# Optimization experiments

Hardware: AMD Instinct MI355X
Metric: run time of the kernel (lower is better)

Reference implementation:

```python
import jax, jax.numpy as jnp
from jax import lax
import numpy as np

B, CIN, HC, K, REC = 64, 64, 64, 3, 5
MG = 240 // REC  # 48
EPS = 1e-8


def conv2d(x, w, b, pad):
    y = lax.conv_general_dilated(x, w, (1, 1), [(pad, pad), (pad, pad)],
                                 dimension_numbers=('NCHW', 'OIHW', 'NCHW'))
    return y + b[None, :, None, None]


def conv_transpose2d(x, w, b, stride, pad):
    # PyTorch ConvTranspose2d: w is (Cin, Cout, kH, kW)
    k = w.shape[2]
    w_t = jnp.transpose(w[:, :, ::-1, ::-1], (1, 0, 2, 3))  # -> OIHW, flipped
    y = lax.conv_general_dilated(x, w_t, (1, 1),
                                 [(k - 1 - pad, k - 1 - pad)] * 2,
                                 lhs_dilation=(stride, stride),
                                 dimension_numbers=('NCHW', 'OIHW', 'NCHW'))
    return y + b[None, :, None, None]


def leaky(x):
    return jnp.where(x >= 0, x, 0.2 * x)


def setup_inputs() -> dict:
    key = jax.random.key(0)
    ks = jax.random.split(key, 12)
    s = 0.05
    return {
        'x': jax.random.normal(ks[0], (B, CIN, 64, 64), jnp.float32),
        'h': jax.random.normal(ks[1], (B, HC, 64, 64), jnp.float32),
        'c': jax.random.normal(ks[2], (B, HC, 64, 64), jnp.float32),
        'recalled_memory_feature': jax.random.normal(ks[3], (B, REC, MG, 32, 32), jnp.float32),
        'conv_w': jax.random.normal(ks[4], (5 * HC, CIN + HC, K, K), jnp.float32) * s,
        'conv_b': jax.random.normal(ks[5], (5 * HC,), jnp.float32) * s,
        'convc_w': jax.random.normal(ks[6], (MG, HC, 1, 1), jnp.float32) * s,
        'convc_b': jax.random.normal(ks[7], (MG,), jnp.float32) * s,
        'convssm_w': jax.random.normal(ks[8], (MG, MG, 4, 4), jnp.float32) * s,
        'convssm_b': jax.random.normal(ks[9], (MG,), jnp.float32) * s,
        'convfuse_w': jax.random.normal(ks[10], (HC, MG + HC, 1, 1), jnp.float32) * s,
        'convfuse_b': jax.random.normal(ks[11], (HC,), jnp.float32) * s,
    }


def reference(x, h, c, recalled_memory_feature, conv_w, conv_b, convc_w, convc_b,
              convssm_w, convssm_b, convfuse_w, convfuse_b):
    rm = recalled_memory_feature.reshape(B, REC, MG, 32, 32)
    rm_avg = rm.mean(axis=(3, 4))                      # (B, REC, MG)
    q = leaky(conv2d(c, convc_w, convc_b, 0))          # (B, MG, 64, 64)
    q_avg = q.mean(axis=(2, 3))                        # (B, MG)
    # cosine similarity along channel dim, vectorized over (B, REC)
    qn = jnp.maximum(jnp.linalg.norm(q_avg, axis=1, keepdims=True), EPS)   # (B,1)
    mn = jnp.maximum(jnp.linalg.norm(rm_avg, axis=2), EPS)                  # (B,REC)
    cos = jnp.einsum('bm,brm->br', q_avg, rm_avg) / (qn * mn)               # (B,REC)
    attn = jax.nn.softmax(cos, axis=1)                                      # (B,REC)
    mt = jnp.einsum('br,brmhw->bmhw', attn, rm)        # (B, MG, 32, 32)
    mt = leaky(conv_transpose2d(mt, convssm_w, convssm_b, 2, 1))  # (B, MG, 64, 64)

    gates = conv2d(jnp.concatenate((x, h), axis=1), conv_w, conv_b, K // 2)
    i, f, g, o, lam = jnp.split(gates, 5, axis=1)
    i = jax.nn.sigmoid(i)
    f = jax.nn.sigmoid(f)
    o = jax.nn.sigmoid(o)
    g = jnp.tanh(g)
    lam = jax.nn.sigmoid(lam)
    c_new = f * c + i * g
    h_new = o * jnp.tanh(conv2d(jnp.concatenate((c_new, mt), axis=1), convfuse_w, convfuse_b, 0))
    h_out = lam * h_new + (1.0 - lam) * h
    return (h_out, c_new)
```

## Files before the change

### kernel.cpp

```cpp
#include <hip/hip_runtime.h>
#include <hip/hip_bf16.h>
#include <cstdint>

#define HW 4096
#define MGc 48
#define RECc 5

typedef __attribute__((ext_vector_type(8))) short bf16x8;
typedef __attribute__((ext_vector_type(4))) float f32x4;

__device__ __forceinline__ float sigf(float x) { return 1.f / (1.f + expf(-x)); }
__device__ __forceinline__ float leakyf(float x) { return x >= 0.f ? x : 0.2f * x; }
__device__ __forceinline__ unsigned short f2bfu(float f) {
  __hip_bfloat16 b = __float2bfloat16(f);
  return *reinterpret_cast<unsigned short*>(&b);
}
__device__ __forceinline__ float bfu2f(unsigned short u) {
  unsigned v = ((unsigned)u) << 16;
  return __uint_as_float(v);
}
__device__ __forceinline__ void gload_lds16(const void* g, void* l) {
  __builtin_amdgcn_global_load_lds(
      (const __attribute__((address_space(1))) unsigned int*)g,
      (__attribute__((address_space(3))) unsigned int*)l, 16, 0, 0);
}

__global__ __launch_bounds__(256) void k_att(const float* __restrict__ rm,
    float* __restrict__ rm_sum, const float* __restrict__ c,
    const float* __restrict__ ccw, const float* __restrict__ ccb,
    float* __restrict__ q_part) {
  __shared__ __align__(16) char smem[13568];
  int bid = blockIdx.x, tid = threadIdx.x;
  if (bid < 15360) {
    float* sred = (float*)smem;
    int row = bid;
    const float4* p = reinterpret_cast<const float4*>(rm + (size_t)row * 1024);
    float4 v = p[tid];
    float s = v.x + v.y + v.z + v.w;
    #pragma unroll
    for (int off = 32; off; off >>= 1) s += __shfl_down(s, off);
    if ((tid & 63) == 0) sred[tid >> 6] = s;
    __syncthreads();
    if (tid == 0) rm_sum[row] = sred[0] + sred[1] + sred[2] + sred[3];
  } else {
    float* wl = (float*)smem;
    float* bl = wl + MGc * 64;
    float (*red)[MGc] = (float(*)[MGc])(bl + 64);
    int r = bid - 15360;
    int seg = r & 15, b = r >> 4;
    for (int i = tid; i < MGc * 64; i += 256) wl[i] = ccw[i];
    if (tid < MGc) bl[tid] = ccb[tid];
    __syncthreads();
    int px = seg * 256 + tid;
    float acc[MGc];
    #pragma unroll
    for (int m = 0; m < MGc; m++) acc[m] = 0.f;
    const float* cp = c + (size_t)b * 64 * HW + px;
    for (int ci = 0; ci < 64; ci++) {
      float v = cp[(size_t)ci * HW];
      #pragma unroll
      for (int m = 0; m < MGc; m++) acc[m] += wl[m * 64 + ci] * v;
    }
    int lane = tid & 63, wv = tid >> 6;
    #pragma unroll
    for (int m = 0; m < MGc; m++) {
      float t2 = leakyf(acc[m] + bl[m]);
      #pragma unroll
      for (int off = 32; off; off >>= 1) t2 += __shfl_down(t2, off);
      if (lane == 0) red[wv][m] = t2;
    }
    __syncthreads();
    if (tid < MGc) {
      float t2 = red[0][tid] + red[1][tid] + red[2][tid] + red[3][tid];
      q_part[((size_t)b * 16 + seg) * MGc + tid] = t2;
    }
  }
}

__global__ __launch_bounds__(256) void k_mid(const float* __restrict__ rm,
    const float* __restrict__ rm_sum, const float* __restrict__ q_part,
    float* __restrict__ mt_pre, const float* __restrict__ cw,
    __hip_bfloat16* __restrict__ Wp, __hip_bfloat16* __restrict__ Pp,
    const float* __restrict__ xin, const float* __restrict__ hin) {
  __shared__ __align__(16) char smem[16704];
  int bid = blockIdx.x, tid = threadIdx.x;
  if (bid < 12288) {
    float* sat = (float*)smem;
    int idx = bid * 256 + tid;
    int b = idx / (MGc * 1024);
    if (tid < 64) {
      int lane = tid;
      float q = 0.f;
      if (lane < MGc) {
        float s = 0.f;
        for (int sg = 0; sg < 16; sg++) s += q_part[((size_t)b * 16 + sg) * MGc + lane];
        q = s * (1.f / 4096.f);
      }
      float qs = q * q;
      #pragma unroll
      for (int off = 32; off; off >>= 1) qs += __shfl_xor(qs, off);
      float qn = fmaxf(sqrtf(qs), 1e-8f);
      float cosv[RECc];
      #pragma unroll
      for (int r = 0; r < RECc; r++) {
        float m = 0.f;
        if (lane < MGc) m = rm_sum[((size_t)b * RECc + r) * MGc + lane] * (1.f / 1024.f);
        float d = q * m, ms = m * m;
        #pragma unroll
        for (int off = 32; off; off >>= 1) { d += __shfl_xor(d, off); ms += __shfl_xor(ms, off); }
        float mn = fmaxf(sqrtf(ms), 1e-8f);
        cosv[r] = d / (qn * mn);
      }
      float mx = cosv[0];
      #pragma unroll
      for (int r = 1; r < RECc; r++) mx = fmaxf(mx, cosv[r]);
      float ssum = 0.f;
      #pragma unroll
      for (int r = 0; r < RECc; r++) { cosv[r] = expf(cosv[r] - mx); ssum += cosv[r]; }
      float inv = 1.f / ssum;
      #pragma unroll
      for (int r = 0; r < RECc; r++)
        if (lane == r) sat[r] = cosv[r] * inv;
    }
    __syncthreads();
    int rem = idx - b * (MGc * 1024);
    const float* base = rm + (size_t)b * RECc * MGc * 1024 + rem;
    float v = sat[0] * base[0] + sat[1] * base[MGc * 1024] + sat[2] * base[2 * MGc * 1024]
            + sat[3] * base[3 * MGc * 1024] + sat[4] * base[4 * MGc * 1024];
    mt_pre[idx] = v;
  } else if (bid < 13728) {
    int idx = (bid - 12288) * 256 + tid;
    int t = idx / (320 * 128);
    int rem = idx % (320 * 128);
    int ocp = rem / 128, ci = rem % 128;
    int nt = ocp / 80, r2 = ocp % 80, gate = r2 / 16, ml = r2 % 16;
    int oc = gate * 64 + nt * 16 + ml;
    Wp[idx] = __float2bfloat16(cw[((size_t)oc * 128 + ci) * 9 + t]);
  } else if (bid < 14768) {
    int idx = (bid - 13728) * 256 + tid;
    int b = idx / 4160, i = idx % 4160;
    bf16x8* base = reinterpret_cast<bf16x8*>(Pp);
    size_t u;
    if (i < 2112) {
      int r = (i < 1056) ? 0 : 65;
      int j = (i < 1056) ? i : i - 1056;
      u = ((size_t)b * 66 + r) * 1056 + j;
    } else {
      int i2 = i - 2112;
      int row = 1 + (i2 >> 5), k = i2 & 31;
      int px = (k < 16) ? 0 : 65, ci8 = k & 15;
      u = (((size_t)b * 66 + row) * 66 + px) * 16 + ci8;
    }
    base[u] = (bf16x8)0;
  } else {
    float (*t)[65] = (float(*)[65])smem;
    int r = bid - 14768;
    int half = r & 1, y = (r >> 1) & 63, b = r >> 7;
    const float* src = (half ? hin : xin) + (size_t)b * 64 * HW + y * 64;
    #pragma unroll
    for (int it = 0; it < 4; it++) {
      int li = it * 256 + tid;
      int ci = li >> 4, x4 = (li & 15) * 4;
      float4 v = *reinterpret_cast<const float4*>(src + (size_t)ci * HW + x4);
      t[x4][ci] = v.x; t[x4 + 1][ci] = v.y; t[x4 + 2][ci] = v.z; t[x4 + 3][ci] = v.w;
    }
    __syncthreads();
    int x = tid >> 2, c16 = (tid & 3) * 16;
    unsigned short* dst = reinterpret_cast<unsigned short*>(Pp) +
        ((((size_t)b * 66 + y + 1) * 66 + x + 1) * 128 + half * 64 + c16);
    bf16x8 o0, o1;
    #pragma unroll
    for (int j = 0; j < 8; j++) {
      o0[j] = (short)f2bfu(t[x][c16 + j]);
      o1[j] = (short)f2bfu(t[x][c16 + 8 + j]);
    }
    *reinterpret_cast<bf16x8*>(dst) = o0;
    *reinterpret_cast<bf16x8*>(dst + 8) = o1;
  }
}

__global__ __launch_bounds__(512) void k_ssm(const float* __restrict__ mt_pre,
    const float* __restrict__ w, const float* __restrict__ bias,
    __hip_bfloat16* __restrict__ mt) {
  __shared__ float in_t[12][10][20];
  __shared__ float w_t[12][48][16];
  int b = blockIdx.y;
  int tile = blockIdx.x;
  int y0 = (tile >> 1) * 16, x0 = (tile & 1) * 32;
  int wv = threadIdx.x >> 6, lane = threadIdx.x & 63;
  int co0 = wv * 6;
  int oyl = lane >> 2, xseg = lane & 3;
  int oy = y0 + oyl;
  int iy0 = (y0 >> 1) - 1, ix0 = (x0 >> 1) - 1;
  int kyA = (oy + 1) & 1;
  int iyA = (oy + 1 - kyA) >> 1;
  int rA = iyA - iy0, rB = rA - 1;
  float acc[6][8] = {};
  for (int ch = 0; ch < 4; ch++) {
    int ci0 = ch * 12;
    __syncthreads();
    for (int i = threadIdx.x; i < 12 * 10 * 18; i += 512) {
      int ci = i / 180, rr = (i % 180) / 18, cc2 = i % 18;
      int giy = iy0 + rr, gix = ix0 + cc2;
      float v = 0.f;
      if ((unsigned)giy < 32u && (unsigned)gix < 32u)
        v = mt_pre[(((size_t)b * MGc + ci0 + ci) * 32 + giy) * 32 + gix];
      in_t[ci][rr][cc2] = v;
    }
    for (int i = threadIdx.x; i < 12 * 48 * 16; i += 512)
      (&w_t[0][0][0])[i] = w[ci0 * 768 + i];
    __syncthreads();
    #pragma unroll 1
    for (int ci = 0; ci < 12; ci++) {
      float4 a0 = *reinterpret_cast<const float4*>(&in_t[ci][rA][xseg * 4]);
      float4 a1 = *reinterpret_cast<const float4*>(&in_t[ci][rA][xseg * 4 + 4]);
      float4 b0 = *reinterpret_cast<const float4*>(&in_t[ci][rB][xseg * 4]);
      float4 b1 = *reinterpret_cast<const float4*>(&in_t[ci][rB][xseg * 4 + 4]);
      float vA[6] = {a0.x, a0.y, a0.z, a0.w, a1.x, a1.y};
      float vB[6] = {b0.x, b0.y, b0.z, b0.w, b1.x, b1.y};
      #pragma unroll
      for (int co = 0; co < 6; co++) {
        const float* wp = &w_t[ci][co0 + co][0];
        float4 wA = *reinterpret_cast<const float4*>(wp + kyA * 4);
        float4 wB = *reinterpret_cast<const float4*>(wp + (kyA + 2) * 4);
        #pragma unroll
        for (int j = 0; j < 8; j++) {
          if ((j & 1) == 0) {
            int hi = (j >> 1) + 1, lo = j >> 1;
            acc[co][j] += vA[hi] * wA.y + vA[lo] * wA.w + vB[hi] * wB.y + vB[lo] * wB.w;
          } else {
            int hi = ((j + 1) >> 1) + 1, lo = (j + 1) >> 1;
            acc[co][j] += vA[hi] * wA.x + vA[lo] * wA.z + vB[hi] * wB.x + vB[lo] * wB.z;
          }
        }
      }
    }
  }
  int oxb = x0 + xseg * 8;
  #pragma unroll
  for (int co = 0; co < 6; co++) {
    float bb = bias[co0 + co];
    size_t obase = (((size_t)b * MGc + co0 + co) * 64 + oy) * 64 + oxb;
    #pragma unroll
    for (int j = 0; j < 8; j++)
      mt[obase + j] = __float2bfloat16(leakyf(acc[co][j] + bb));
  }
}

__global__ __launch_bounds__(256) void k_gates_mfma(
    const __hip_bfloat16* __restrict__ Pp, const __hip_bfloat16* __restrict__ Wp,
    const float* __restrict__ c, const float* __restrict__ cb,
    float* __restrict__ c_new, __hip_bfloat16* __restrict__ o_g,
    __hip_bfloat16* __restrict__ lam_g) {
  __shared__ bf16x8 s_in[1296];
  __shared__ bf16x8 s_w[2944];
  int orig = blockIdx.y * gridDim.x + blockIdx.x;
  int t_id = (orig & 7) * 512 + (orig >> 3);
  int b = t_id >> 6;
  int r6 = t_id & 63;
  int ytile = r6 >> 4, xtile = (r6 >> 2) & 3, nt = r6 & 3;
  int y0 = ytile * 16, x0 = xtile * 16;
  int tid = threadIdx.x;
  int wv = tid >> 6, lane = tid & 63;
  int lane15 = lane & 15, lq = lane >> 4;

  const char* Pb = (const char*)Pp;
  const char* Wb = (const char*)Wp;

  const char* gin[6]; int din[6]; bool ain[6];
  #pragma unroll
  for (int k = 0; k < 6; k++) {
    int u = wv + 4 * k;
    int e = u * 64 + lane;
    ain[k] = (u < 21) && (e < 1296);
    int ee = (e < 1296) ? e : 0;
    int L = ee / 72, r = ee - L * 72;
    int llq = r / 18, xi = r - llq * 18;
    gin[k] = Pb + ((((size_t)b * 66 + y0 + L) * 66 + (x0 + xi)) * 256) + llq * 16;
    din[k] = ee;
  }
  const char* gw[12]; int dw[12]; bool aw[12];
  #pragma unroll
  for (int k = 0; k < 12; k++) {
    int u = wv + 4 * k;
    int e = u * 64 + lane;
    aw[k] = (e < 2916);
    int ee = aw[k] ? e : 0;
    int row = ee / 81, ol = ee - row * 81;
    if (ol > 79) ol = 0;
    int t = row >> 2, g = row & 3;
    gw[k] = Wb + (((size_t)t * 320 + nt * 80 + ol) * 128 + g * 8) * 2;
    dw[k] = ee;
  }

  f32x4 acc[4][5];
  #pragma unroll
  for (int i = 0; i < 4; i++)
    #pragma unroll
    for (int j = 0; j < 5; j++) acc[i][j] = (f32x4)0.f;

  #pragma unroll 1
  for (int cc = 0; cc < 4; cc++) {
    __syncthreads();
    int co = cc * 64;
    #pragma unroll
    for (int k = 0; k < 6; k++)
      if (ain[k]) gload_lds16(gin[k] + co, (void*)&s_in[din[k]]);
    #pragma unroll
    for (int k = 0; k < 12; k++)
      if (aw[k]) gload_lds16(gw[k] + co, (void*)&s_w[dw[k]]);
    __syncthreads();

    #pragma unroll
    for (int dx = 0; dx < 3; dx++) {
      bf16x8 af[6];
      #pragma unroll
      for (int r = 0; r < 6; r++)
        af[r] = s_in[((wv * 4 + r) * 4 + lq) * 18 + lane15 + dx];
      #pragma unroll
      for (int ky = 0; ky < 3; ky++) {
        int t = ky * 3 + dx;
        bf16x8 bw[5];
        #pragma unroll
        for (int gg = 0; gg < 5; gg++)
          bw[gg] = s_w[(t * 4 + lq) * 81 + gg * 16 + lane15];
        __builtin_amdgcn_s_setprio(1);
        #pragma unroll
        for (int rr = 0; rr < 4; rr++)
          #pragma unroll
          for (int gg = 0; gg < 5; gg++)
            acc[rr][gg] = __builtin_amdgcn_mfma_f32_16x16x32_bf16(
                af[rr + ky], bw[gg], acc[rr][gg], 0, 0, 0);
        __builtin_amdgcn_s_setprio(0);
      }
    }
  }

  int m_hid = nt * 16 + lane15;
  float bi = cb[m_hid], bff = cb[64 + m_hid], bgg = cb[128 + m_hid],
        bo = cb[192 + m_hid], bl = cb[256 + m_hid];
  int xb = x0 + lq * 4;
  size_t chofs = ((size_t)b * 64 + m_hid) * HW;
  #pragma unroll
  for (int rr = 0; rr < 4; rr++) {
    int y = y0 + wv * 4 + rr;
    size_t pofs = chofs + (size_t)y * 64 + xb;
    f32x4 cold = *reinterpret_cast<const f32x4*>(c + pofs);
    f32x4 cn;
    unsigned short ov[4], lv[4];
    #pragma unroll
    for (int e = 0; e < 4; e++) {
      float i_ = sigf(acc[rr][0][e] + bi);
      float f_ = sigf(acc[rr][1][e] + bff);
      float g_ = tanhf(acc[rr][2][e] + bgg);
      float o_ = sigf(acc[rr][3][e] + bo);
      float l_ = sigf(acc[rr][4][e] + bl);
      cn[e] = f_ * cold[e] + i_ * g_;
      ov[e] = f2bfu(o_);
      lv[e] = f2bfu(l_);
    }
    *reinterpret_cast<f32x4*>(c_new + pofs) = cn;
    ushort4 ovv = {ov[0], ov[1], ov[2], ov[3]};
    ushort4 lvv = {lv[0], lv[1], lv[2], lv[3]};
    *reinterpret_cast<ushort4*>(reinterpret_cast<unsigned short*>(o_g) + pofs) = ovv;
    *reinterpret_cast<ushort4*>(reinterpret_cast<unsigned short*>(lam_g) + pofs) = lvv;
  }
}

__global__ __launch_bounds__(256) void k_fuse(const float* __restrict__ c_new,
    const __hip_bfloat16* __restrict__ mt, const __hip_bfloat16* __restrict__ o_g,
    const __hip_bfloat16* __restrict__ lam_g, const float* __restrict__ h,
    const float* __restrict__ fw, const float* __restrict__ fb,
    float* __restrict__ h_out) {
  __shared__ float wl[112][32];
  int b = blockIdx.y;
  int seg = blockIdx.x & 7, chalf = blockIdx.x >> 3;
  int co0 = chalf * 32;
  for (int i = threadIdx.x; i < 112 * 32; i += 256) {
    int ci = i >> 5, co = i & 31;
    wl[ci][co] = fw[(co0 + co) * 112 + ci];
  }
  __syncthreads();
  int px = seg * 512 + threadIdx.x * 2;
  size_t bofs = (size_t)b * 64 * HW;
  float2 acc[32];
  #pragma unroll
  for (int co = 0; co < 32; co++) { float bv = fb[co0 + co]; acc[co].x = bv; acc[co].y = bv; }
  #pragma unroll 1
  for (int ci = 0; ci < 64; ci++) {
    float2 v = *reinterpret_cast<const float2*>(c_new + bofs + (size_t)ci * HW + px);
    #pragma unroll
    for (int c4 = 0; c4 < 8; c4++) {
      float4 w = *reinterpret_cast<const float4*>(&wl[ci][c4 * 4]);
      acc[c4 * 4 + 0].x += w.x * v.x; acc[c4 * 4 + 0].y += w.x * v.y;
      acc[c4 * 4 + 1].x += w.y * v.x; acc[c4 * 4 + 1].y += w.y * v.y;
      acc[c4 * 4 + 2].x += w.z * v.x; acc[c4 * 4 + 2].y += w.z * v.y;
      acc[c4 * 4 + 3].x += w.w * v.x; acc[c4 * 4 + 3].y += w.w * v.y;
    }
  }
  const unsigned short* mtu = reinterpret_cast<const unsigned short*>(mt);
  size_t mtofs = (size_t)b * MGc * HW + px;
  #pragma unroll 1
  for (int ci = 0; ci < 48; ci++) {
    unsigned u = *reinterpret_cast<const unsigned*>(mtu + mtofs + (size_t)ci * HW);
    float vx = bfu2f((unsigned short)(u & 0xffff));
    float vy = bfu2f((unsigned short)(u >> 16));
    #pragma unroll
    for (int c4 = 0; c4 < 8; c4++) {
      float4 w = *reinterpret_cast<const float4*>(&wl[64 + ci][c4 * 4]);
      acc[c4 * 4 + 0].x += w.x * vx; acc[c4 * 4 + 0].y += w.x * vy;
      acc[c4 * 4 + 1].x += w.y * vx; acc[c4 * 4 + 1].y += w.y * vy;
      acc[c4 * 4 + 2].x += w.z * vx; acc[c4 * 4 + 2].y += w.z * vy;
      acc[c4 * 4 + 3].x += w.w * vx; acc[c4 * 4 + 3].y += w.w * vy;
    }
  }
  const unsigned short* ou = reinterpret_cast<const unsigned short*>(o_g);
  const unsigned short* lu = reinterpret_cast<const unsigned short*>(lam_g);
  #pragma unroll
  for (int co = 0; co < 32; co++) {
    size_t ofs = bofs + (size_t)(co0 + co) * HW + px;
    unsigned uo = *reinterpret_cast<const unsigned*>(ou + ofs);
    unsigned ul = *reinterpret_cast<const unsigned*>(lu + ofs);
    float2 hv = *reinterpret_cast<const float2*>(h + ofs);
    float hnx = tanhf(acc[co].x), hny = tanhf(acc[co].y);
    float ox = bfu2f((unsigned short)(uo & 0xffff)), oy = bfu2f((unsigned short)(uo >> 16));
    float lx = bfu2f((unsigned short)(ul & 0xffff)), ly = bfu2f((unsigned short)(ul >> 16));
    float2 r;
    r.x = lx * (ox * hnx) + (1.f - lx) * hv.x;
    r.y = ly * (oy * hny) + (1.f - ly) * hv.y;
    *reinterpret_cast<float2*>(h_out + ofs) = r;
  }
}

extern "C" void kernel_launch(void* const* d_in, const int* in_sizes, int n_in,
                              void* d_out, int out_size, void* d_ws, size_t ws_size,
                              hipStream_t stream) {
  const float* x   = (const float*)d_in[0];
  const float* h   = (const float*)d_in[1];
  const float* c   = (const float*)d_in[2];
  const float* rm  = (const float*)d_in[3];
  const float* cw  = (const float*)d_in[4];
  const float* cb  = (const float*)d_in[5];
  const float* ccw = (const float*)d_in[6];
  const float* ccb = (const float*)d_in[7];
  const float* sw  = (const float*)d_in[8];
  const float* sb  = (const float*)d_in[9];
  const float* fw  = (const float*)d_in[10];
  const float* fb  = (const float*)d_in[11];

  float* h_out = (float*)d_out;
  float* c_new = h_out + (size_t)16777216;

  char* ws = (char*)d_ws;
  float* rm_sum = (float*)(ws + 0);
  float* q_part = (float*)(ws + 65536);
  __hip_bfloat16* o_g   = (__hip_bfloat16*)(ws + 0);
  __hip_bfloat16* lam_g = (__hip_bfloat16*)(ws + 33554432);
  __hip_bfloat16* mt    = (__hip_bfloat16*)(ws + 67108864);
  __hip_bfloat16* Pp    = (__hip_bfloat16*)(ws + 92274688);
  __hip_bfloat16* Wp    = (__hip_bfloat16*)(ws + 163643392);
  float* mt_pre = h_out;

  k_att<<<16384, 256, 0, stream>>>(rm, rm_sum, c, ccw, ccb, q_part);
  k_mid<<<22960, 256, 0, stream>>>(rm, rm_sum, q_part, mt_pre, cw, Wp, Pp, x, h);
  k_ssm<<<dim3(8, 64), 512, 0, stream>>>(mt_pre, sw, sb, mt);
  k_gates_mfma<<<dim3(64, 64), 256, 0, stream>>>(Pp, Wp, c, cb, c_new, o_g, lam_g);
  k_fuse<<<dim3(16, 64), 256, 0, stream>>>(c_new, mt, o_g, lam_g, h, fw, fb, h_out);
}
```

Baseline: 641.4 us.

## Double-buffer gate-conv weight tiles per dx to overlap loads with MFMA

The gate convolution kernel now stages its weight tile one dx column at a time into two 960-entry LDS buffers, instead of loading all nine taps into one large buffer before computing. The global-to-LDS load for the next dx is issued before the MFMA work on the current dx, so weight loads overlap compute. This also cuts LDS use per block, which may allow more resident blocks. In exchange it adds barriers per channel chunk and drops the 81-entry padded row stride for a stride of 80, which may bring back LDS bank conflicts on the B-fragment reads.

```diff
diff --git a/kernel.cpp b/kernel.cpp
--- a/kernel.cpp
+++ b/kernel.cpp
@@ -253,7 +253,7 @@
     float* __restrict__ c_new, __hip_bfloat16* __restrict__ o_g,
     __hip_bfloat16* __restrict__ lam_g) {
   __shared__ bf16x8 s_in[1296];
-  __shared__ bf16x8 s_w[2944];
+  __shared__ bf16x8 s_w[2][960];
   int orig = blockIdx.y * gridDim.x + blockIdx.x;
   int t_id = (orig & 7) * 512 + (orig >> 3);
   int b = t_id >> 6;
@@ -279,18 +279,17 @@
     gin[k] = Pb + ((((size_t)b * 66 + y0 + L) * 66 + (x0 + xi)) * 256) + llq * 16;
     din[k] = ee;
   }
-  const char* gw[12]; int dw[12]; bool aw[12];
-  #pragma unroll
-  for (int k = 0; k < 12; k++) {
+  const char* gwb[4]; int dwb[4]; bool awb[4];
+  #pragma unroll
+  for (int k = 0; k < 4; k++) {
     int u = wv + 4 * k;
-    int e = u * 64 + lane;
-    aw[k] = (e < 2916);
-    int ee = aw[k] ? e : 0;
-    int row = ee / 81, ol = ee - row * 81;
-    if (ol > 79) ol = 0;
-    int t = row >> 2, g = row & 3;
-    gw[k] = Wb + (((size_t)t * 320 + nt * 80 + ol) * 128 + g * 8) * 2;
-    dw[k] = ee;
+    awb[k] = (u < 15);
+    int uu = awb[k] ? u : 0;
+    int e = uu * 64 + lane;
+    int row = e / 80, ol = e - row * 80;
+    int ky = row >> 2, g = row & 3;
+    gwb[k] = Wb + (((size_t)(ky * 3) * 320 + nt * 80 + ol) * 128 + g * 8) * 2;
+    dwb[k] = e;
   }
 
   f32x4 acc[4][5];
@@ -298,43 +297,55 @@
   for (int i = 0; i < 4; i++)
     #pragma unroll
     for (int j = 0; j < 5; j++) acc[i][j] = (f32x4)0.f;
+
+#define STAGE_W(BUF, DX, CO) do {                                                     \
+    _Pragma("unroll")                                                                 \
+    for (int k = 0; k < 4; k++)                                                       \
+      if (awb[k]) gload_lds16(gwb[k] + (DX) * 81920 + (CO),                           \
+                              (void*)&s_w[BUF][dwb[k]]);                              \
+  } while (0)
+
+#define COMP_DX(BUF, DX) do {                                                         \
+    bf16x8 af[6];                                                                     \
+    _Pragma("unroll")                                                                 \
+    for (int r = 0; r < 6; r++)                                                       \
+      af[r] = s_in[((wv * 4 + r) * 4 + lq) * 18 + lane15 + (DX)];                     \
+    _Pragma("unroll")                                                                 \
+    for (int ky = 0; ky < 3; ky++) {                                                  \
+      bf16x8 bw[5];                                                                   \
+      _Pragma("unroll")                                                               \
+      for (int gg = 0; gg < 5; gg++)                                                  \
+        bw[gg] = s_w[BUF][(ky * 4 + lq) * 80 + gg * 16 + lane15];                     \
+      __builtin_amdgcn_s_setprio(1);                                                  \
+      _Pragma("unroll")                                                               \
+      for (int rr = 0; rr < 4; rr++)                                                  \
+        _Pragma("unroll")                                                             \
+        for (int gg = 0; gg < 5; gg++)                                                \
+          acc[rr][gg] = __builtin_amdgcn_mfma_f32_16x16x32_bf16(                      \
+              af[rr + ky], bw[gg], acc[rr][gg], 0, 0, 0);                             \
+      __builtin_amdgcn_s_setprio(0);                                                  \
+    }                                                                                 \
+  } while (0)
 
   #pragma unroll 1
   for (int cc = 0; cc < 4; cc++) {
-    __syncthreads();
     int co = cc * 64;
+    __syncthreads();
     #pragma unroll
     for (int k = 0; k < 6; k++)
       if (ain[k]) gload_lds16(gin[k] + co, (void*)&s_in[din[k]]);
-    #pragma unroll
-    for (int k = 0; k < 12; k++)
-      if (aw[k]) gload_lds16(gw[k] + co, (void*)&s_w[dw[k]]);
-    __syncthreads();
-
-    #pragma unroll
-    for (int dx = 0; dx < 3; dx++) {
-      bf16x8 af[6];
-      #pragma unroll
-      for (int r = 0; r < 6; r++)
-        af[r] = s_in[((wv * 4 + r) * 4 + lq) * 18 + lane15 + dx];
-      #pragma unroll
-      for (int ky = 0; ky < 3; ky++) {
-        int t = ky * 3 + dx;
-        bf16x8 bw[5];
-        #pragma unroll
-        for (int gg = 0; gg < 5; gg++)
-          bw[gg] = s_w[(t * 4 + lq) * 81 + gg * 16 + lane15];
-        __builtin_amdgcn_s_setprio(1);
-        #pragma unroll
-        for (int rr = 0; rr < 4; rr++)
-          #pragma unroll
-          for (int gg = 0; gg < 5; gg++)
-            acc[rr][gg] = __builtin_amdgcn_mfma_f32_16x16x32_bf16(
-                af[rr + ky], bw[gg], acc[rr][gg], 0, 0, 0);
-        __builtin_amdgcn_s_setprio(0);
-      }
-    }
-  }
+    STAGE_W(0, 0, co);
+    __syncthreads();
+    STAGE_W(1, 1, co);
+    COMP_DX(0, 0);
+    __syncthreads();
+    STAGE_W(0, 2, co);
+    COMP_DX(1, 1);
+    __syncthreads();
+    COMP_DX(0, 2);
+  }
+#undef STAGE_W
+#undef COMP_DX
 
   int m_hid = nt * 16 + lane15;
   float bi = cb[m_hid], bff = cb[64 + m_hid], bgg = cb[128 + m_hid],
```

Result: no change. 629.2 us (-1.9%).
